# Kernel optimization log

Measured on AMD Instinct MI355X. Metric: run time of the kernel, lower is better.

Reference implementation:

```python
import jax, jax.numpy as jnp
import numpy as np
import math

N_HEAD = 16

def setup_inputs() -> dict:
    key = jax.random.key(0)
    ks = jax.random.split(key, 5)
    B, T, C = 4, 2048, 1024
    x = jax.random.normal(ks[0], (B, T, C), dtype=jnp.float32)
    # xavier-uniform-ish scale for dense kernels
    W_attn = jax.random.normal(ks[1], (C, 3 * C), dtype=jnp.float32) * (1.0 / math.sqrt(C))
    b_attn = jnp.zeros((3 * C,), dtype=jnp.float32)
    W_proj = jax.random.normal(ks[2], (C, C), dtype=jnp.float32) * (1.0 / math.sqrt(C))
    b_proj = jnp.zeros((C,), dtype=jnp.float32)
    return {"x": x, "W_attn": W_attn, "b_attn": b_attn, "W_proj": W_proj, "b_proj": b_proj}

def reference(x, W_attn, b_attn, W_proj, b_proj):
    B, T, C = x.shape
    H = N_HEAD
    D = C // H
    qkv = x @ W_attn + b_attn                      # [B,T,3C]
    q, k, v = jnp.split(qkv, 3, axis=-1)
    q = q.reshape(B, T, H, D).transpose(0, 2, 1, 3)  # [B,H,T,D]
    k = k.reshape(B, T, H, D).transpose(0, 2, 1, 3)
    v = v.reshape(B, T, H, D).transpose(0, 2, 1, 3)
    att = jnp.einsum("bhqd,bhkd->bhqk", q, k) * (1.0 / math.sqrt(D))  # [B,H,T,T]
    causal = jnp.tril(jnp.ones((T, T), dtype=bool))
    att = jnp.where(causal, att, jnp.float32(-jnp.inf))
    att = jax.nn.softmax(att, axis=-1)             # exp(att - logsumexp)
    # dropout rates are 0.0 -> identity
    y = jnp.einsum("bhqk,bhkd->bhqd", att, v)      # [B,H,T,D]
    y = y.transpose(0, 2, 1, 3).reshape(B, T, C)
    y = y @ W_proj + b_proj
    return y
```

## Files before the change

kernel.cpp:

```cpp
#include <hip/hip_runtime.h>
#include <hip/hip_bf16.h>

typedef short s16x8 __attribute__((ext_vector_type(8)));
typedef float f32x4 __attribute__((ext_vector_type(4)));
typedef float f32x2 __attribute__((ext_vector_type(2)));

#define MFMA_BF16(A, B, C) __builtin_amdgcn_mfma_f32_16x16x32_bf16(A, B, C, 0, 0, 0)

constexpr int Bn = 4, Tn = 2048, Cn = 1024, Hn = 16, Dn = 64;
constexpr int Mn = Bn * Tn;
constexpr int Nqkv = 3 * Cn;
constexpr float SC = 0.125f * 1.44269504089f;

__device__ __forceinline__ ushort f2bfu(float f) {
    __hip_bfloat16 h = __float2bfloat16(f);
    return *reinterpret_cast<ushort*>(&h);
}
__device__ __forceinline__ uint pkbf(float a, float b) {
    __hip_bfloat162 h = __float22bfloat162_rn(make_float2(a, b));
    return *reinterpret_cast<uint*>(&h);
}

__device__ __forceinline__ f32x2 pk_add(f32x2 a, f32x2 b) {
    f32x2 d; asm("v_pk_add_f32 %0, %1, %2" : "=v"(d) : "v"(a), "v"(b)); return d;
}
__device__ __forceinline__ f32x2 pk_mul(f32x2 a, f32x2 b) {
    f32x2 d; asm("v_pk_mul_f32 %0, %1, %2" : "=v"(d) : "v"(a), "v"(b)); return d;
}

__device__ __forceinline__ void gl_lds16(const void* g, void* l) {
    __builtin_amdgcn_global_load_lds(
        (const __attribute__((address_space(1))) void*)(uintptr_t)g,
        (__attribute__((address_space(3))) void*)(uint32_t)(uintptr_t)l,
        16, 0, 0);
}

__global__ __launch_bounds__(256) void conv_bf16_kernel(
    const float* __restrict__ src, ushort* __restrict__ dst, int n4)
{
    int i = blockIdx.x * blockDim.x + threadIdx.x;
    int stride = gridDim.x * blockDim.x;
    for (; i < n4; i += stride) {
        float4 v = ((const float4*)src)[i];
        ushort4 o;
        o.x = f2bfu(v.x); o.y = f2bfu(v.y); o.z = f2bfu(v.z); o.w = f2bfu(v.w);
        ((ushort4*)dst)[i] = o;
    }
}

__global__ __launch_bounds__(256) void transpose_cvt_kernel(
    const float* __restrict__ W, ushort* __restrict__ Wt, int K, int N)
{
    __shared__ __align__(16) float Ls[64][68];
    const int t = threadIdx.x;
    const int n0 = blockIdx.x * 64, k0 = blockIdx.y * 64;
#pragma unroll
    for (int p = 0; p < 4; ++p) {
        int r = (t >> 4) + p * 16;
        int c = (t & 15) * 4;
        *(float4*)&Ls[r][c] = *(const float4*)&W[(size_t)(k0 + r) * N + n0 + c];
    }
    __syncthreads();
    const int n = t >> 2;
    const int ks = (t & 3) * 16;
    union { ushort s[16]; uint4 u[2]; } tmp;
#pragma unroll
    for (int j = 0; j < 16; ++j) tmp.s[j] = f2bfu(Ls[ks + j][n]);
    uint4* dp = (uint4*)&Wt[(size_t)(n0 + n) * K + k0 + ks];
    dp[0] = tmp.u[0];
    dp[1] = tmp.u[1];
}

__global__ __launch_bounds__(256) void vt_transpose_kernel(
    const ushort* __restrict__ V, ushort* __restrict__ Vt)
{
    const int tid = threadIdx.x;
    const int bh = blockIdx.x;
    const int kt0 = blockIdx.y * 64;
    const ushort* src = V + (size_t)bh * Tn * Dn;
    ushort* dst = Vt + (size_t)bh * Dn * Tn;
    const int vk = (tid & 15) * 4, vd = (tid >> 4) * 4;
    const ushort* g = src + (size_t)(kt0 + vk) * Dn + vd;
    ushort4 v0 = *(const ushort4*)(g);
    ushort4 v1 = *(const ushort4*)(g + Dn);
    ushort4 v2 = *(const ushort4*)(g + 2 * Dn);
    ushort4 v3 = *(const ushort4*)(g + 3 * Dn);
    ushort4 t0, t1, t2, t3;
    t0.x = v0.x; t0.y = v1.x; t0.z = v2.x; t0.w = v3.x;
    t1.x = v0.y; t1.y = v1.y; t1.z = v2.y; t1.w = v3.y;
    t2.x = v0.z; t2.y = v1.z; t2.z = v2.z; t2.w = v3.z;
    t3.x = v0.w; t3.y = v1.w; t3.z = v2.w; t3.w = v3.w;
    *(ushort4*)(dst + (size_t)(vd + 0) * Tn + kt0 + vk) = t0;
    *(ushort4*)(dst + (size_t)(vd + 1) * Tn + kt0 + vk) = t1;
    *(ushort4*)(dst + (size_t)(vd + 2) * Tn + kt0 + vk) = t2;
    *(ushort4*)(dst + (size_t)(vd + 3) * Tn + kt0 + vk) = t3;
}

__global__ __launch_bounds__(256) void qkv_gemm_mfma(
    const ushort* __restrict__ A, const ushort* __restrict__ Bt,
    const float* __restrict__ bias,
    ushort* __restrict__ Qo, ushort* __restrict__ Ko, ushort* __restrict__ Vo)
{
    __shared__ __align__(16) ushort As[128 * 64];
    __shared__ __align__(16) ushort Bs[128 * 64];
    const int tid = threadIdx.x;
    const int m0 = blockIdx.x * 128, n0 = blockIdx.y * 128;
    const int w = tid >> 6, lane = tid & 63, l15 = lane & 15, qd = lane >> 4;
    const int wm = (w >> 1) * 64, wn = (w & 1) * 64;
    const int lrow = lane >> 3;
    const int lchunk = (lane & 7) ^ (lrow & 7);

    const ushort* gA = A + (size_t)(m0 + w * 32 + lrow) * Cn + lchunk * 8;
    const ushort* gB = Bt + (size_t)(n0 + w * 32 + lrow) * Cn + lchunk * 8;
    ushort* lA = &As[(w * 32) * 64];
    ushort* lB = &Bs[(w * 32) * 64];

    f32x4 acc[4][4] = {};

    for (int k0 = 0; k0 < Cn; k0 += 64) {
        __syncthreads();
#pragma unroll
        for (int t = 0; t < 4; ++t) {
            gl_lds16(gA + (size_t)t * 8 * Cn + k0, lA + t * 8 * 64);
            gl_lds16(gB + (size_t)t * 8 * Cn + k0, lB + t * 8 * 64);
        }
        __syncthreads();
#pragma unroll
        for (int ks = 0; ks < 2; ++ks) {
            const int xs = (((ks * 4 + qd) ^ (l15 & 7))) * 8;
            s16x8 af[4], bfr[4];
#pragma unroll
            for (int i = 0; i < 4; ++i) {
                af[i]  = *(const s16x8*)&As[(wm + i * 16 + l15) * 64 + xs];
                bfr[i] = *(const s16x8*)&Bs[(wn + i * 16 + l15) * 64 + xs];
            }
#pragma unroll
            for (int mt = 0; mt < 4; ++mt)
#pragma unroll
                for (int nt = 0; nt < 4; ++nt)
                    acc[mt][nt] = MFMA_BF16(af[mt], bfr[nt], acc[mt][nt]);
        }
    }

#pragma unroll
    for (int nt = 0; nt < 4; ++nt) {
        int n_g = n0 + wn + nt * 16 + l15;
        float bv = bias[n_g];
        int sel = n_g >> 10;
        int h = (n_g >> 6) & 15;
        int d = n_g & 63;
        ushort* O = (sel == 0) ? Qo : ((sel == 1) ? Ko : Vo);
        float scl = (sel == 0) ? SC : 1.0f;
#pragma unroll
        for (int mt = 0; mt < 4; ++mt) {
#pragma unroll
            for (int r = 0; r < 4; ++r) {
                int m_g = m0 + wm + mt * 16 + qd * 4 + r;
                int b = m_g >> 11, t = m_g & 2047;
                O[(((size_t)(b * Hn + h) * Tn + t) << 6) + d] =
                    f2bfu((acc[mt][nt][r] + bv) * scl);
            }
        }
    }
}

__global__ __launch_bounds__(256, 4) void attn_mfma(
    const ushort* __restrict__ Q, const ushort* __restrict__ K,
    const ushort* __restrict__ Vt, ushort* __restrict__ Y)
{
    __shared__ __align__(16) ushort Ks[2][64 * 64];
    __shared__ __align__(16) ushort Vs[2][64 * 64];
    __shared__ __align__(16) ushort Ps[64 * 64];

    const int tid = threadIdx.x;
    const int bh = blockIdx.x, bx = blockIdx.y;
    const int w = tid >> 6, lane = tid & 63, l15 = lane & 15, qd = lane >> 4;
    const size_t base = (size_t)bh * Tn * Dn;
    const int lrow = lane >> 3;
    const int lchunk = (lane & 7) ^ (lrow & 7);
    const int q_l = w * 16 + l15;
    const int frow = (w * 16 + l15) * 64;
    const int fx0 = ((0 * 4 + qd) ^ (l15 & 7)) * 8;
    const int fx1 = ((1 * 4 + qd) ^ (l15 & 7)) * 8;
    const int b = bh >> 4, h = bh & 15;

    const ushort* Kg = K + base + (size_t)(w * 16 + lrow) * Dn + lchunk * 8;
    const ushort* Vg = Vt + base + (size_t)(w * 16 + lrow) * Tn + lchunk * 8;
    const ushort* Qp = Q + base + (size_t)l15 * Dn + qd * 8;

#pragma unroll
    for (int half = 0; half < 2; ++half) {
        const int qt = half ? (31 - bx) : bx;

        const ushort* qrow = Qp + (size_t)(qt * 64 + w * 16) * Dn;
        s16x8 qf0 = *(const s16x8*)(qrow);
        s16x8 qf1 = *(const s16x8*)(qrow + 32);

        __syncthreads();
#pragma unroll
        for (int t = 0; t < 2; ++t) {
            gl_lds16(Kg + (size_t)(t * 8) * Dn, &Ks[0][(w * 16 + t * 8) * 64]);
            gl_lds16(Vg + (size_t)(t * 8) * Tn, &Vs[0][(w * 16 + t * 8) * 64]);
        }

        float m_run = -1e30f, l_run = 0.f;
        f32x4 o[4] = {};

        for (int kt = 0; kt <= qt; ++kt) {
            const int buf = kt & 1;
            __syncthreads();
            if (kt < qt) {
#pragma unroll
                for (int t = 0; t < 2; ++t) {
                    gl_lds16(Kg + (size_t)((kt + 1) * 64 + t * 8) * Dn,
                             &Ks[buf ^ 1][(w * 16 + t * 8) * 64]);
                    gl_lds16(Vg + (size_t)(t * 8) * Tn + (kt + 1) * 64,
                             &Vs[buf ^ 1][(w * 16 + t * 8) * 64]);
                }
            }

            f32x4 s[4] = {};
#pragma unroll
            for (int nt = 0; nt < 4; ++nt) {
                s16x8 kf = *(const s16x8*)&Ks[buf][(nt * 16 + l15) * 64 + fx0];
                s[nt] = MFMA_BF16(kf, qf0, s[nt]);
            }
#pragma unroll
            for (int nt = 0; nt < 4; ++nt) {
                s16x8 kf = *(const s16x8*)&Ks[buf][(nt * 16 + l15) * 64 + fx1];
                s[nt] = MFMA_BF16(kf, qf1, s[nt]);
            }

            if (kt == qt) {
#pragma unroll
                for (int nt = 0; nt < 4; ++nt)
#pragma unroll
                    for (int r = 0; r < 4; ++r)
                        if (nt * 16 + qd * 4 + r > q_l) s[nt][r] = -1e30f;
            }

            float a0 = fmaxf(fmaxf(s[0][0], s[0][1]), fmaxf(s[0][2], s[0][3]));
            float a1 = fmaxf(fmaxf(s[1][0], s[1][1]), fmaxf(s[1][2], s[1][3]));
            float a2 = fmaxf(fmaxf(s[2][0], s[2][1]), fmaxf(s[2][2], s[2][3]));
            float a3 = fmaxf(fmaxf(s[3][0], s[3][1]), fmaxf(s[3][2], s[3][3]));
            float mx = fmaxf(fmaxf(a0, a1), fmaxf(a2, a3));
            mx = fmaxf(mx, __shfl_xor(mx, 16));
            mx = fmaxf(mx, __shfl_xor(mx, 32));

            if (!__all(mx <= m_run + 8.f)) {
                float m_new = fmaxf(m_run, mx);
                float alpha = exp2f(m_run - m_new);
                m_run = m_new;
                l_run *= alpha;
                f32x2 aa = {alpha, alpha};
#pragma unroll
                for (int dt = 0; dt < 4; ++dt) {
                    o[dt].lo = pk_mul(o[dt].lo, aa);
                    o[dt].hi = pk_mul(o[dt].hi, aa);
                }
            }

            const f32x2 negm = {-m_run, -m_run};
            f32x2 lac0 = {0.f, 0.f}, lac1 = {0.f, 0.f};
#pragma unroll
            for (int nt = 0; nt < 4; ++nt) {
                s[nt].lo = pk_add(s[nt].lo, negm);
                s[nt].hi = pk_add(s[nt].hi, negm);
                s[nt][0] = exp2f(s[nt][0]);
                s[nt][1] = exp2f(s[nt][1]);
                s[nt][2] = exp2f(s[nt][2]);
                s[nt][3] = exp2f(s[nt][3]);
                lac0 = pk_add(lac0, s[nt].lo);
                lac1 = pk_add(lac1, s[nt].hi);
            }
            lac0 = pk_add(lac0, lac1);
            l_run += lac0[0] + lac0[1];

#pragma unroll
            for (int nt = 0; nt < 4; ++nt) {
                uint2 pk;
                pk.x = pkbf(s[nt][0], s[nt][1]);
                pk.y = pkbf(s[nt][2], s[nt][3]);
                const int pc = 2 * nt + (qd >> 1), po = (qd & 1) * 4;
                *(uint2*)&Ps[frow + ((pc ^ (l15 & 7)) * 8) + po] = pk;
            }

            {
                s16x8 pb = *(const s16x8*)&Ps[frow + fx0];
#pragma unroll
                for (int dt = 0; dt < 4; ++dt) {
                    s16x8 vf = *(const s16x8*)&Vs[buf][(dt * 16 + l15) * 64 + fx0];
                    o[dt] = MFMA_BF16(vf, pb, o[dt]);
                }
                pb = *(const s16x8*)&Ps[frow + fx1];
#pragma unroll
                for (int dt = 0; dt < 4; ++dt) {
                    s16x8 vf = *(const s16x8*)&Vs[buf][(dt * 16 + l15) * 64 + fx1];
                    o[dt] = MFMA_BF16(vf, pb, o[dt]);
                }
            }
        }

        float lt = l_run;
        lt += __shfl_xor(lt, 16);
        lt += __shfl_xor(lt, 32);
        const float inv = 1.f / lt;
        const int t_g = qt * 64 + w * 16 + l15;
        ushort* yp = Y + ((size_t)(b * Tn + t_g)) * Cn + h * Dn + qd * 4;
#pragma unroll
        for (int dt = 0; dt < 4; ++dt) {
            uint2 pk;
            pk.x = pkbf(o[dt][0] * inv, o[dt][1] * inv);
            pk.y = pkbf(o[dt][2] * inv, o[dt][3] * inv);
            *(uint2*)(yp + dt * 16) = pk;
        }
    }
}

__global__ __launch_bounds__(256) void proj_gemm_mfma(
    const ushort* __restrict__ A, const ushort* __restrict__ Bt,
    const float* __restrict__ bias, float* __restrict__ out)
{
    __shared__ __align__(16) ushort As[128 * 64];
    __shared__ __align__(16) ushort Bs[128 * 64];
    const int tid = threadIdx.x;
    const int m0 = blockIdx.x * 128, n0 = blockIdx.y * 128;
    const int w = tid >> 6, lane = tid & 63, l15 = lane & 15, qd = lane >> 4;
    const int wm = (w >> 1) * 64, wn = (w & 1) * 64;
    const int lrow = lane >> 3;
    const int lchunk = (lane & 7) ^ (lrow & 7);

    const ushort* gA = A + (size_t)(m0 + w * 32 + lrow) * Cn + lchunk * 8;
    const ushort* gB = Bt + (size_t)(n0 + w * 32 + lrow) * Cn + lchunk * 8;
    ushort* lA = &As[(w * 32) * 64];
    ushort* lB = &Bs[(w * 32) * 64];

    f32x4 acc[4][4] = {};

    for (int k0 = 0; k0 < Cn; k0 += 64) {
        __syncthreads();
#pragma unroll
        for (int t = 0; t < 4; ++t) {
            gl_lds16(gA + (size_t)t * 8 * Cn + k0, lA + t * 8 * 64);
            gl_lds16(gB + (size_t)t * 8 * Cn + k0, lB + t * 8 * 64);
        }
        __syncthreads();
#pragma unroll
        for (int ks = 0; ks < 2; ++ks) {
            const int xs = (((ks * 4 + qd) ^ (l15 & 7))) * 8;
            s16x8 af[4], bfr[4];
#pragma unroll
            for (int i = 0; i < 4; ++i) {
                af[i]  = *(const s16x8*)&As[(wm + i * 16 + l15) * 64 + xs];
                bfr[i] = *(const s16x8*)&Bs[(wn + i * 16 + l15) * 64 + xs];
            }
#pragma unroll
            for (int mt = 0; mt < 4; ++mt)
#pragma unroll
                for (int nt = 0; nt < 4; ++nt)
                    acc[mt][nt] = MFMA_BF16(af[mt], bfr[nt], acc[mt][nt]);
        }
    }

#pragma unroll
    for (int nt = 0; nt < 4; ++nt) {
        int n_g = n0 + wn + nt * 16 + l15;
        float bv = bias[n_g];
#pragma unroll
        for (int mt = 0; mt < 4; ++mt) {
#pragma unroll
            for (int r = 0; r < 4; ++r) {
                int m_g = m0 + wm + mt * 16 + qd * 4 + r;
                out[(size_t)m_g * Cn + n_g] = acc[mt][nt][r] + bv;
            }
        }
    }
}

extern "C" void kernel_launch(void* const* d_in, const int* in_sizes, int n_in,
                              void* d_out, int out_size, void* d_ws, size_t ws_size,
                              hipStream_t stream) {
    const float* x      = (const float*)d_in[0];
    const float* W_attn = (const float*)d_in[1];
    const float* b_attn = (const float*)d_in[2];
    const float* W_proj = (const float*)d_in[3];
    const float* b_proj = (const float*)d_in[4];
    float* out = (float*)d_out;

    constexpr size_t PER = (size_t)Mn * Cn;
    ushort* Qb = (ushort*)d_ws;
    ushort* Kb = Qb + PER;
    ushort* Vb = Kb + PER;
    ushort* Yb = Vb + PER;

    ushort* WtA  = (ushort*)d_out;
    ushort* x_bf = WtA + (size_t)Nqkv * Cn;
    ushort* Vtb  = (ushort*)d_out;
    ushort* WtP  = Qb;

    conv_bf16_kernel<<<1024, 256, 0, stream>>>(x, x_bf, (int)(PER / 4));
    transpose_cvt_kernel<<<dim3(Nqkv / 64, Cn / 64), 256, 0, stream>>>(
        W_attn, WtA, Cn, Nqkv);
    qkv_gemm_mfma<<<dim3(Mn / 128, Nqkv / 128), 256, 0, stream>>>(
        x_bf, WtA, b_attn, Qb, Kb, Vb);
    vt_transpose_kernel<<<dim3(Bn * Hn, Tn / 64), 256, 0, stream>>>(Vb, Vtb);
    attn_mfma<<<dim3(Bn * Hn, 16), 256, 0, stream>>>(Qb, Kb, Vtb, Yb);
    transpose_cvt_kernel<<<dim3(Cn / 64, Cn / 64), 256, 0, stream>>>(
        W_proj, WtP, Cn, Cn);
    proj_gemm_mfma<<<dim3(Mn / 128, Cn / 128), 256, 0, stream>>>(
        Yb, WtP, b_proj, out);
}
```

Before: 264.4 us.

## Process two adjacent query tiles per attention block sharing K/V loads

Each attention block now handles two adjacent 64-row query tiles (128 rows) in a single pass over the K/V tiles. Before, it ran two separate passes for a complementary pair of tiles (bx and 31-bx). Sharing the K/V stream halves global and LDS traffic per query row and removes the second loop's prologue. The per-tile softmax and PV step is factored into a helper, and blockIdx.y is permuted within groups of eight. In exchange, the balanced pairing is lost, so block work now grows with j. Holding two sets of accumulators and Q fragments raises register pressure under the 4-waves launch bound.

```diff
diff --git a/kernel.cpp b/kernel.cpp
--- a/kernel.cpp
+++ b/kernel.cpp
@@ -164,6 +164,73 @@
     }
 }
 
+__device__ __forceinline__ void sm_pv(
+    f32x4 (&s)[4], float& m_run, float& l_run, f32x4 (&o)[4],
+    const ushort* __restrict__ Vsb, ushort* __restrict__ Pr,
+    int fx0, int fx1, int l15, int qd)
+{
+    float a0 = fmaxf(fmaxf(s[0][0], s[0][1]), fmaxf(s[0][2], s[0][3]));
+    float a1 = fmaxf(fmaxf(s[1][0], s[1][1]), fmaxf(s[1][2], s[1][3]));
+    float a2 = fmaxf(fmaxf(s[2][0], s[2][1]), fmaxf(s[2][2], s[2][3]));
+    float a3 = fmaxf(fmaxf(s[3][0], s[3][1]), fmaxf(s[3][2], s[3][3]));
+    float mx = fmaxf(fmaxf(a0, a1), fmaxf(a2, a3));
+    mx = fmaxf(mx, __shfl_xor(mx, 16));
+    mx = fmaxf(mx, __shfl_xor(mx, 32));
+
+    if (!__all(mx <= m_run + 8.f)) {
+        float m_new = fmaxf(m_run, mx);
+        float alpha = exp2f(m_run - m_new);
+        m_run = m_new;
+        l_run *= alpha;
+        f32x2 aa = {alpha, alpha};
+#pragma unroll
+        for (int dt = 0; dt < 4; ++dt) {
+            o[dt].lo = pk_mul(o[dt].lo, aa);
+            o[dt].hi = pk_mul(o[dt].hi, aa);
+        }
+    }
+
+    const f32x2 negm = {-m_run, -m_run};
+    f32x2 lac0 = {0.f, 0.f}, lac1 = {0.f, 0.f};
+#pragma unroll
+    for (int nt = 0; nt < 4; ++nt) {
+        s[nt].lo = pk_add(s[nt].lo, negm);
+        s[nt].hi = pk_add(s[nt].hi, negm);
+        s[nt][0] = exp2f(s[nt][0]);
+        s[nt][1] = exp2f(s[nt][1]);
+        s[nt][2] = exp2f(s[nt][2]);
+        s[nt][3] = exp2f(s[nt][3]);
+        lac0 = pk_add(lac0, s[nt].lo);
+        lac1 = pk_add(lac1, s[nt].hi);
+    }
+    lac0 = pk_add(lac0, lac1);
+    l_run += lac0[0] + lac0[1];
+
+#pragma unroll
+    for (int nt = 0; nt < 4; ++nt) {
+        uint2 pk;
+        pk.x = pkbf(s[nt][0], s[nt][1]);
+        pk.y = pkbf(s[nt][2], s[nt][3]);
+        const int pc = 2 * nt + (qd >> 1), po = (qd & 1) * 4;
+        *(uint2*)&Pr[((pc ^ (l15 & 7)) * 8) + po] = pk;
+    }
+
+    {
+        s16x8 pb = *(const s16x8*)&Pr[fx0];
+#pragma unroll
+        for (int dt = 0; dt < 4; ++dt) {
+            s16x8 vf = *(const s16x8*)&Vsb[(dt * 16 + l15) * 64 + fx0];
+            o[dt] = MFMA_BF16(vf, pb, o[dt]);
+        }
+        pb = *(const s16x8*)&Pr[fx1];
+#pragma unroll
+        for (int dt = 0; dt < 4; ++dt) {
+            s16x8 vf = *(const s16x8*)&Vsb[(dt * 16 + l15) * 64 + fx1];
+            o[dt] = MFMA_BF16(vf, pb, o[dt]);
+        }
+    }
+}
+
 __global__ __launch_bounds__(256, 4) void attn_mfma(
     const ushort* __restrict__ Q, const ushort* __restrict__ K,
     const ushort* __restrict__ Vt, ushort* __restrict__ Y)
@@ -173,145 +240,129 @@
     __shared__ __align__(16) ushort Ps[64 * 64];
 
     const int tid = threadIdx.x;
-    const int bh = blockIdx.x, bx = blockIdx.y;
+    const int bh = blockIdx.x;
+    const int y = blockIdx.y;
+    const int j = ((y >> 2) & 1) ? ((y & 8) + 7 - (y & 3)) : y;
     const int w = tid >> 6, lane = tid & 63, l15 = lane & 15, qd = lane >> 4;
     const size_t base = (size_t)bh * Tn * Dn;
     const int lrow = lane >> 3;
     const int lchunk = (lane & 7) ^ (lrow & 7);
     const int q_l = w * 16 + l15;
-    const int frow = (w * 16 + l15) * 64;
-    const int fx0 = ((0 * 4 + qd) ^ (l15 & 7)) * 8;
-    const int fx1 = ((1 * 4 + qd) ^ (l15 & 7)) * 8;
+    const int frow = q_l * 64;
+    const int fx0 = (qd ^ (l15 & 7)) * 8;
+    const int fx1 = ((4 + qd) ^ (l15 & 7)) * 8;
     const int b = bh >> 4, h = bh & 15;
+
+    const int qb = j * 128;
+    const int ktend = 2 * j + 1;
 
     const ushort* Kg = K + base + (size_t)(w * 16 + lrow) * Dn + lchunk * 8;
     const ushort* Vg = Vt + base + (size_t)(w * 16 + lrow) * Tn + lchunk * 8;
     const ushort* Qp = Q + base + (size_t)l15 * Dn + qd * 8;
 
-#pragma unroll
-    for (int half = 0; half < 2; ++half) {
-        const int qt = half ? (31 - bx) : bx;
-
-        const ushort* qrow = Qp + (size_t)(qt * 64 + w * 16) * Dn;
-        s16x8 qf0 = *(const s16x8*)(qrow);
-        s16x8 qf1 = *(const s16x8*)(qrow + 32);
-
+    const ushort* qrowA = Qp + (size_t)(qb + w * 16) * Dn;
+    const ushort* qrowB = Qp + (size_t)(qb + 64 + w * 16) * Dn;
+    s16x8 qfA0 = *(const s16x8*)(qrowA);
+    s16x8 qfA1 = *(const s16x8*)(qrowA + 32);
+    s16x8 qfB0 = *(const s16x8*)(qrowB);
+    s16x8 qfB1 = *(const s16x8*)(qrowB + 32);
+
+#pragma unroll
+    for (int t = 0; t < 2; ++t) {
+        gl_lds16(Kg + (size_t)(t * 8) * Dn, &Ks[0][(w * 16 + t * 8) * 64]);
+        gl_lds16(Vg + (size_t)(t * 8) * Tn, &Vs[0][(w * 16 + t * 8) * 64]);
+    }
+
+    float mA = -1e30f, lA = 0.f, mB = -1e30f, lB = 0.f;
+    f32x4 oA[4] = {}, oB[4] = {};
+
+    for (int kt = 0; kt <= ktend; ++kt) {
+        const int buf = kt & 1;
         __syncthreads();
-#pragma unroll
-        for (int t = 0; t < 2; ++t) {
-            gl_lds16(Kg + (size_t)(t * 8) * Dn, &Ks[0][(w * 16 + t * 8) * 64]);
-            gl_lds16(Vg + (size_t)(t * 8) * Tn, &Vs[0][(w * 16 + t * 8) * 64]);
-        }
-
-        float m_run = -1e30f, l_run = 0.f;
-        f32x4 o[4] = {};
-
-        for (int kt = 0; kt <= qt; ++kt) {
-            const int buf = kt & 1;
-            __syncthreads();
-            if (kt < qt) {
-#pragma unroll
-                for (int t = 0; t < 2; ++t) {
-                    gl_lds16(Kg + (size_t)((kt + 1) * 64 + t * 8) * Dn,
-                             &Ks[buf ^ 1][(w * 16 + t * 8) * 64]);
-                    gl_lds16(Vg + (size_t)(t * 8) * Tn + (kt + 1) * 64,
-                             &Vs[buf ^ 1][(w * 16 + t * 8) * 64]);
-                }
-            }
-
-            f32x4 s[4] = {};
+        if (kt < ktend) {
+#pragma unroll
+            for (int t = 0; t < 2; ++t) {
+                gl_lds16(Kg + (size_t)((kt + 1) * 64 + t * 8) * Dn,
+                         &Ks[buf ^ 1][(w * 16 + t * 8) * 64]);
+                gl_lds16(Vg + (size_t)(t * 8) * Tn + (kt + 1) * 64,
+                         &Vs[buf ^ 1][(w * 16 + t * 8) * 64]);
+            }
+        }
+
+        const bool actA = (kt <= 2 * j);
+
+        f32x4 sA[4] = {}, sB[4] = {};
+        if (actA) {
 #pragma unroll
             for (int nt = 0; nt < 4; ++nt) {
                 s16x8 kf = *(const s16x8*)&Ks[buf][(nt * 16 + l15) * 64 + fx0];
-                s[nt] = MFMA_BF16(kf, qf0, s[nt]);
+                sA[nt] = MFMA_BF16(kf, qfA0, sA[nt]);
             }
 #pragma unroll
             for (int nt = 0; nt < 4; ++nt) {
                 s16x8 kf = *(const s16x8*)&Ks[buf][(nt * 16 + l15) * 64 + fx1];
-                s[nt] = MFMA_BF16(kf, qf1, s[nt]);
-            }
-
-            if (kt == qt) {
+                sA[nt] = MFMA_BF16(kf, qfA1, sA[nt]);
+            }
+        }
+#pragma unroll
+        for (int nt = 0; nt < 4; ++nt) {
+            s16x8 kf = *(const s16x8*)&Ks[buf][(nt * 16 + l15) * 64 + fx0];
+            sB[nt] = MFMA_BF16(kf, qfB0, sB[nt]);
+        }
+#pragma unroll
+        for (int nt = 0; nt < 4; ++nt) {
+            s16x8 kf = *(const s16x8*)&Ks[buf][(nt * 16 + l15) * 64 + fx1];
+            sB[nt] = MFMA_BF16(kf, qfB1, sB[nt]);
+        }
+
+        if (actA) {
+            if (kt == 2 * j) {
 #pragma unroll
                 for (int nt = 0; nt < 4; ++nt)
 #pragma unroll
                     for (int r = 0; r < 4; ++r)
-                        if (nt * 16 + qd * 4 + r > q_l) s[nt][r] = -1e30f;
-            }
-
-            float a0 = fmaxf(fmaxf(s[0][0], s[0][1]), fmaxf(s[0][2], s[0][3]));
-            float a1 = fmaxf(fmaxf(s[1][0], s[1][1]), fmaxf(s[1][2], s[1][3]));
-            float a2 = fmaxf(fmaxf(s[2][0], s[2][1]), fmaxf(s[2][2], s[2][3]));
-            float a3 = fmaxf(fmaxf(s[3][0], s[3][1]), fmaxf(s[3][2], s[3][3]));
-            float mx = fmaxf(fmaxf(a0, a1), fmaxf(a2, a3));
-            mx = fmaxf(mx, __shfl_xor(mx, 16));
-            mx = fmaxf(mx, __shfl_xor(mx, 32));
-
-            if (!__all(mx <= m_run + 8.f)) {
-                float m_new = fmaxf(m_run, mx);
-                float alpha = exp2f(m_run - m_new);
-                m_run = m_new;
-                l_run *= alpha;
-                f32x2 aa = {alpha, alpha};
-#pragma unroll
-                for (int dt = 0; dt < 4; ++dt) {
-                    o[dt].lo = pk_mul(o[dt].lo, aa);
-                    o[dt].hi = pk_mul(o[dt].hi, aa);
-                }
-            }
-
-            const f32x2 negm = {-m_run, -m_run};
-            f32x2 lac0 = {0.f, 0.f}, lac1 = {0.f, 0.f};
-#pragma unroll
-            for (int nt = 0; nt < 4; ++nt) {
-                s[nt].lo = pk_add(s[nt].lo, negm);
-                s[nt].hi = pk_add(s[nt].hi, negm);
-                s[nt][0] = exp2f(s[nt][0]);
-                s[nt][1] = exp2f(s[nt][1]);
-                s[nt][2] = exp2f(s[nt][2]);
-                s[nt][3] = exp2f(s[nt][3]);
-                lac0 = pk_add(lac0, s[nt].lo);
-                lac1 = pk_add(lac1, s[nt].hi);
-            }
-            lac0 = pk_add(lac0, lac1);
-            l_run += lac0[0] + lac0[1];
-
-#pragma unroll
-            for (int nt = 0; nt < 4; ++nt) {
-                uint2 pk;
-                pk.x = pkbf(s[nt][0], s[nt][1]);
-                pk.y = pkbf(s[nt][2], s[nt][3]);
-                const int pc = 2 * nt + (qd >> 1), po = (qd & 1) * 4;
-                *(uint2*)&Ps[frow + ((pc ^ (l15 & 7)) * 8) + po] = pk;
-            }
-
-            {
-                s16x8 pb = *(const s16x8*)&Ps[frow + fx0];
-#pragma unroll
-                for (int dt = 0; dt < 4; ++dt) {
-                    s16x8 vf = *(const s16x8*)&Vs[buf][(dt * 16 + l15) * 64 + fx0];
-                    o[dt] = MFMA_BF16(vf, pb, o[dt]);
-                }
-                pb = *(const s16x8*)&Ps[frow + fx1];
-#pragma unroll
-                for (int dt = 0; dt < 4; ++dt) {
-                    s16x8 vf = *(const s16x8*)&Vs[buf][(dt * 16 + l15) * 64 + fx1];
-                    o[dt] = MFMA_BF16(vf, pb, o[dt]);
-                }
-            }
-        }
-
-        float lt = l_run;
+                        if (nt * 16 + qd * 4 + r > q_l) sA[nt][r] = -1e30f;
+            }
+            sm_pv(sA, mA, lA, oA, &Vs[buf][0], &Ps[frow], fx0, fx1, l15, qd);
+        }
+
+        if (kt == ktend) {
+#pragma unroll
+            for (int nt = 0; nt < 4; ++nt)
+#pragma unroll
+                for (int r = 0; r < 4; ++r)
+                    if (nt * 16 + qd * 4 + r > q_l) sB[nt][r] = -1e30f;
+        }
+        sm_pv(sB, mB, lB, oB, &Vs[buf][0], &Ps[frow], fx0, fx1, l15, qd);
+    }
+
+    {
+        float lt = lA;
         lt += __shfl_xor(lt, 16);
         lt += __shfl_xor(lt, 32);
         const float inv = 1.f / lt;
-        const int t_g = qt * 64 + w * 16 + l15;
+        const int t_g = qb + q_l;
         ushort* yp = Y + ((size_t)(b * Tn + t_g)) * Cn + h * Dn + qd * 4;
 #pragma unroll
         for (int dt = 0; dt < 4; ++dt) {
             uint2 pk;
-            pk.x = pkbf(o[dt][0] * inv, o[dt][1] * inv);
-            pk.y = pkbf(o[dt][2] * inv, o[dt][3] * inv);
+            pk.x = pkbf(oA[dt][0] * inv, oA[dt][1] * inv);
+            pk.y = pkbf(oA[dt][2] * inv, oA[dt][3] * inv);
+            *(uint2*)(yp + dt * 16) = pk;
+        }
+    }
+    {
+        float lt = lB;
+        lt += __shfl_xor(lt, 16);
+        lt += __shfl_xor(lt, 32);
+        const float inv = 1.f / lt;
+        const int t_g = qb + 64 + q_l;
+        ushort* yp = Y + ((size_t)(b * Tn + t_g)) * Cn + h * Dn + qd * 4;
+#pragma unroll
+        for (int dt = 0; dt < 4; ++dt) {
+            uint2 pk;
+            pk.x = pkbf(oB[dt][0] * inv, oB[dt][1] * inv);
+            pk.y = pkbf(oB[dt][2] * inv, oB[dt][3] * inv);
             *(uint2*)(yp + dt * 16) = pk;
         }
     }
```

Result: slower. 277.4 us (+4.9%).

## Load V fragments directly from global in attention; vectorize QKV epilogue stores

Applied to the files above, without the earlier changes.

In the attention kernel the V tile is no longer staged through double-buffered LDS. Each lane loads its V^T fragments straight from global memory into registers, split into two halves issued early in the iteration. This cuts LDS usage, so launch bounds rise to five blocks per CU. The QKV GEMM swaps its MFMA operands so each lane holds four consecutive output columns, allowing a float4 bias load and packed 8-byte bf16 stores instead of scalar 2-byte stores. The risk is that uncached global V loads, which each wave repeats, expose latency and add redundant traffic to L2.

```diff
diff --git a/kernel.cpp b/kernel.cpp
--- a/kernel.cpp
+++ b/kernel.cpp
@@ -138,38 +138,38 @@
             for (int mt = 0; mt < 4; ++mt)
 #pragma unroll
                 for (int nt = 0; nt < 4; ++nt)
-                    acc[mt][nt] = MFMA_BF16(af[mt], bfr[nt], acc[mt][nt]);
+                    acc[nt][mt] = MFMA_BF16(bfr[nt], af[mt], acc[nt][mt]);
         }
     }
 
 #pragma unroll
     for (int nt = 0; nt < 4; ++nt) {
-        int n_g = n0 + wn + nt * 16 + l15;
-        float bv = bias[n_g];
-        int sel = n_g >> 10;
-        int h = (n_g >> 6) & 15;
-        int d = n_g & 63;
+        const int n_b = n0 + wn + nt * 16 + qd * 4;
+        const float4 bv = *(const float4*)&bias[n_b];
+        const int sel = n_b >> 10;
+        const int h = (n_b >> 6) & 15;
+        const int d = n_b & 63;
         ushort* O = (sel == 0) ? Qo : ((sel == 1) ? Ko : Vo);
-        float scl = (sel == 0) ? SC : 1.0f;
+        const float scl = (sel == 0) ? SC : 1.0f;
 #pragma unroll
         for (int mt = 0; mt < 4; ++mt) {
-#pragma unroll
-            for (int r = 0; r < 4; ++r) {
-                int m_g = m0 + wm + mt * 16 + qd * 4 + r;
-                int b = m_g >> 11, t = m_g & 2047;
-                O[(((size_t)(b * Hn + h) * Tn + t) << 6) + d] =
-                    f2bfu((acc[mt][nt][r] + bv) * scl);
-            }
-        }
-    }
-}
-
-__global__ __launch_bounds__(256, 4) void attn_mfma(
+            const int m_g = m0 + wm + mt * 16 + l15;
+            const int b = m_g >> 11, t = m_g & 2047;
+            uint2 pk;
+            pk.x = pkbf((acc[nt][mt][0] + bv.x) * scl,
+                        (acc[nt][mt][1] + bv.y) * scl);
+            pk.y = pkbf((acc[nt][mt][2] + bv.z) * scl,
+                        (acc[nt][mt][3] + bv.w) * scl);
+            *(uint2*)&O[(((size_t)(b * Hn + h) * Tn + t) << 6) + d] = pk;
+        }
+    }
+}
+
+__global__ __launch_bounds__(256, 5) void attn_mfma(
     const ushort* __restrict__ Q, const ushort* __restrict__ K,
     const ushort* __restrict__ Vt, ushort* __restrict__ Y)
 {
     __shared__ __align__(16) ushort Ks[2][64 * 64];
-    __shared__ __align__(16) ushort Vs[2][64 * 64];
     __shared__ __align__(16) ushort Ps[64 * 64];
 
     const int tid = threadIdx.x;
@@ -179,13 +179,13 @@
     const int lrow = lane >> 3;
     const int lchunk = (lane & 7) ^ (lrow & 7);
     const int q_l = w * 16 + l15;
-    const int frow = (w * 16 + l15) * 64;
+    const int frow = q_l * 64;
     const int fx0 = ((0 * 4 + qd) ^ (l15 & 7)) * 8;
     const int fx1 = ((1 * 4 + qd) ^ (l15 & 7)) * 8;
     const int b = bh >> 4, h = bh & 15;
 
     const ushort* Kg = K + base + (size_t)(w * 16 + lrow) * Dn + lchunk * 8;
-    const ushort* Vg = Vt + base + (size_t)(w * 16 + lrow) * Tn + lchunk * 8;
+    const ushort* Vg = Vt + base + (size_t)l15 * Tn + qd * 8;
     const ushort* Qp = Q + base + (size_t)l15 * Dn + qd * 8;
 
 #pragma unroll
@@ -198,10 +198,8 @@
 
         __syncthreads();
 #pragma unroll
-        for (int t = 0; t < 2; ++t) {
+        for (int t = 0; t < 2; ++t)
             gl_lds16(Kg + (size_t)(t * 8) * Dn, &Ks[0][(w * 16 + t * 8) * 64]);
-            gl_lds16(Vg + (size_t)(t * 8) * Tn, &Vs[0][(w * 16 + t * 8) * 64]);
-        }
 
         float m_run = -1e30f, l_run = 0.f;
         f32x4 o[4] = {};
@@ -211,13 +209,15 @@
             __syncthreads();
             if (kt < qt) {
 #pragma unroll
-                for (int t = 0; t < 2; ++t) {
+                for (int t = 0; t < 2; ++t)
                     gl_lds16(Kg + (size_t)((kt + 1) * 64 + t * 8) * Dn,
                              &Ks[buf ^ 1][(w * 16 + t * 8) * 64]);
-                    gl_lds16(Vg + (size_t)(t * 8) * Tn + (kt + 1) * 64,
-                             &Vs[buf ^ 1][(w * 16 + t * 8) * 64]);
-                }
-            }
+            }
+
+            s16x8 vf0[4];
+#pragma unroll
+            for (int dt = 0; dt < 4; ++dt)
+                vf0[dt] = *(const s16x8*)(Vg + (size_t)(dt * 16) * Tn + kt * 64);
 
             f32x4 s[4] = {};
 #pragma unroll
@@ -246,6 +246,12 @@
             float mx = fmaxf(fmaxf(a0, a1), fmaxf(a2, a3));
             mx = fmaxf(mx, __shfl_xor(mx, 16));
             mx = fmaxf(mx, __shfl_xor(mx, 32));
+
+            s16x8 vf1[4];
+#pragma unroll
+            for (int dt = 0; dt < 4; ++dt)
+                vf1[dt] = *(const s16x8*)(Vg + (size_t)(dt * 16) * Tn +
+                                          kt * 64 + 32);
 
             if (!__all(mx <= m_run + 8.f)) {
                 float m_new = fmaxf(m_run, mx);
@@ -288,16 +294,12 @@
             {
                 s16x8 pb = *(const s16x8*)&Ps[frow + fx0];
 #pragma unroll
-                for (int dt = 0; dt < 4; ++dt) {
-                    s16x8 vf = *(const s16x8*)&Vs[buf][(dt * 16 + l15) * 64 + fx0];
-                    o[dt] = MFMA_BF16(vf, pb, o[dt]);
-                }
+                for (int dt = 0; dt < 4; ++dt)
+                    o[dt] = MFMA_BF16(vf0[dt], pb, o[dt]);
                 pb = *(const s16x8*)&Ps[frow + fx1];
 #pragma unroll
-                for (int dt = 0; dt < 4; ++dt) {
-                    s16x8 vf = *(const s16x8*)&Vs[buf][(dt * 16 + l15) * 64 + fx1];
-                    o[dt] = MFMA_BF16(vf, pb, o[dt]);
-                }
+                for (int dt = 0; dt < 4; ++dt)
+                    o[dt] = MFMA_BF16(vf1[dt], pb, o[dt]);
             }
         }
 
```

Result: slower. 356.0 us (+34.6%).

## Transpose QKV GEMM MFMA output for packed stores and raise priority around attention MFMAs

Applied to the files above, without the earlier changes.

The QKV projection now swaps the MFMA operands, so each lane holds four consecutive head-dim values for one token. That lets the epilogue load the bias as a float4 and write 8-byte packed bf16 stores instead of scattered 2-byte stores. The attention kernel wraps its QK and PV MFMA sections in s_setprio so those waves get higher issue priority while other waves do softmax work. The risk is that the priority hint does little, or upsets how waves interleave.

```diff
diff --git a/kernel.cpp b/kernel.cpp
--- a/kernel.cpp
+++ b/kernel.cpp
@@ -138,28 +138,29 @@
             for (int mt = 0; mt < 4; ++mt)
 #pragma unroll
                 for (int nt = 0; nt < 4; ++nt)
-                    acc[mt][nt] = MFMA_BF16(af[mt], bfr[nt], acc[mt][nt]);
+                    acc[nt][mt] = MFMA_BF16(bfr[nt], af[mt], acc[nt][mt]);
         }
     }
 
 #pragma unroll
     for (int nt = 0; nt < 4; ++nt) {
-        int n_g = n0 + wn + nt * 16 + l15;
-        float bv = bias[n_g];
-        int sel = n_g >> 10;
-        int h = (n_g >> 6) & 15;
-        int d = n_g & 63;
+        const int n_b = n0 + wn + nt * 16 + qd * 4;
+        const float4 bv = *(const float4*)&bias[n_b];
+        const int sel = n_b >> 10;
+        const int h = (n_b >> 6) & 15;
+        const int d = n_b & 63;
         ushort* O = (sel == 0) ? Qo : ((sel == 1) ? Ko : Vo);
-        float scl = (sel == 0) ? SC : 1.0f;
+        const float scl = (sel == 0) ? SC : 1.0f;
 #pragma unroll
         for (int mt = 0; mt < 4; ++mt) {
-#pragma unroll
-            for (int r = 0; r < 4; ++r) {
-                int m_g = m0 + wm + mt * 16 + qd * 4 + r;
-                int b = m_g >> 11, t = m_g & 2047;
-                O[(((size_t)(b * Hn + h) * Tn + t) << 6) + d] =
-                    f2bfu((acc[mt][nt][r] + bv) * scl);
-            }
+            const int m_g = m0 + wm + mt * 16 + l15;
+            const int b = m_g >> 11, t = m_g & 2047;
+            uint2 pk;
+            pk.x = pkbf((acc[nt][mt][0] + bv.x) * scl,
+                        (acc[nt][mt][1] + bv.y) * scl);
+            pk.y = pkbf((acc[nt][mt][2] + bv.z) * scl,
+                        (acc[nt][mt][3] + bv.w) * scl);
+            *(uint2*)&O[(((size_t)(b * Hn + h) * Tn + t) << 6) + d] = pk;
         }
     }
 }
@@ -179,7 +180,7 @@
     const int lrow = lane >> 3;
     const int lchunk = (lane & 7) ^ (lrow & 7);
     const int q_l = w * 16 + l15;
-    const int frow = (w * 16 + l15) * 64;
+    const int frow = q_l * 64;
     const int fx0 = ((0 * 4 + qd) ^ (l15 & 7)) * 8;
     const int fx1 = ((1 * 4 + qd) ^ (l15 & 7)) * 8;
     const int b = bh >> 4, h = bh & 15;
@@ -220,6 +221,7 @@
             }
 
             f32x4 s[4] = {};
+            __builtin_amdgcn_s_setprio(1);
 #pragma unroll
             for (int nt = 0; nt < 4; ++nt) {
                 s16x8 kf = *(const s16x8*)&Ks[buf][(nt * 16 + l15) * 64 + fx0];
@@ -230,6 +232,7 @@
                 s16x8 kf = *(const s16x8*)&Ks[buf][(nt * 16 + l15) * 64 + fx1];
                 s[nt] = MFMA_BF16(kf, qf1, s[nt]);
             }
+            __builtin_amdgcn_s_setprio(0);
 
             if (kt == qt) {
 #pragma unroll
@@ -287,6 +290,7 @@
 
             {
                 s16x8 pb = *(const s16x8*)&Ps[frow + fx0];
+                __builtin_amdgcn_s_setprio(1);
 #pragma unroll
                 for (int dt = 0; dt < 4; ++dt) {
                     s16x8 vf = *(const s16x8*)&Vs[buf][(dt * 16 + l15) * 64 + fx0];
@@ -298,6 +302,7 @@
                     s16x8 vf = *(const s16x8*)&Vs[buf][(dt * 16 + l15) * 64 + fx1];
                     o[dt] = MFMA_BF16(vf, pb, o[dt]);
                 }
+                __builtin_amdgcn_s_setprio(0);
             }
         }
 
```

Measured after the change: 273.4 us. 1.03x slower.
